# Kernel optimization log

Hardware: AMD Instinct MI355X
Metric: run time of the kernel (lower is better)

Reference implementation:

```python
import jax, jax.numpy as jnp
import numpy as np

B, L, D = 4, 1024, 1024
H = 16
HD = D // H
SCALE = HD ** -0.5
LOCAL_WINDOW = 32
HALF = LOCAL_WINDOW // 2
TEMP = 1.0
PATTERN_TEMP = 1.0
THRESHOLD = 0.1
SPARSITY_RATIO = 0.3
# k for learned sparse topk (eval mode, static given L)
EFF = min(SPARSITY_RATIO, 1.0 - 10.0 / L)
K_TOP = max(1, min(L, int(L * (1.0 - EFF))))


def setup_inputs() -> dict:
    key = jax.random.key(0)
    ks = jax.random.split(key, 16)
    def xavier(k, shape, gain=1.0):
        fan_in, fan_out = shape[1], shape[0]
        a = gain * np.sqrt(6.0 / (fan_in + fan_out))
        return jax.random.uniform(k, shape, jnp.float32, -a, a)
    return {
        'x': jax.random.normal(ks[0], (B, L, D), jnp.float32),
        'w_qkv': xavier(ks[1], (3 * D, D), gain=1.0 / np.sqrt(2.0)),
        'w_proj': xavier(ks[2], (D, D)),
        'b_proj': jnp.zeros((D,), jnp.float32),
        'ps_w1': xavier(ks[3], (D, D), gain=0.5),
        'ps_b1': jnp.zeros((D,), jnp.float32),
        'ln_g': jnp.ones((D,), jnp.float32),
        'ln_b': jnp.zeros((D,), jnp.float32),
        'ps_w2': xavier(ks[4], (D // 2, D), gain=0.5),
        'ps_b2': jnp.zeros((D // 2,), jnp.float32),
        'ps_w3': xavier(ks[5], (3, D // 2), gain=0.5),
        'ps_b3': jnp.zeros((3,), jnp.float32),
        'pattern_bias': jnp.array([0.05, 0.0, -0.05], jnp.float32),
        'sparse_w': jax.random.normal(ks[6], (H, 1, 1), jnp.float32) * 0.1 + 1.0,
        'sparse_b': jnp.zeros((H, 1, 1), jnp.float32),
    }


def _forward(x, w_qkv, w_proj, b_proj, ps_w1, ps_b1, ln_g, ln_b,
             ps_w2, ps_b2, ps_w3, ps_b3, pattern_bias, sparse_w, sparse_b):
    qkv = (x @ w_qkv.T).reshape(B, L, 3, H, HD)
    qkv = jnp.transpose(qkv, (2, 0, 3, 1, 4))  # [3,B,H,L,HD]
    q, k, v = qkv[0], qkv[1], qkv[2]
    scores = jnp.einsum('bhid,bhjd->bhij', q, k) * SCALE  # [B,H,L,L]

    # pattern selector on pooled features
    pooled = (jnp.mean(x, axis=1) + jnp.max(x, axis=1)) / 2.0  # [B,D]
    h = pooled @ ps_w1.T + ps_b1
    mu = jnp.mean(h, axis=-1, keepdims=True)
    var = jnp.mean((h - mu) ** 2, axis=-1, keepdims=True)
    h = (h - mu) / jnp.sqrt(var + 1e-5) * ln_g + ln_b
    h = jax.nn.gelu(h, approximate=False)
    h = jax.nn.gelu(h @ ps_w2.T + ps_b2, approximate=False)
    logits = h @ ps_w3.T + ps_b3 + pattern_bias  # [B,3]
    pw = jax.nn.softmax(logits / PATTERN_TEMP, axis=-1)  # [B,3]

    # learned sparse mask via per-head affine + topk scatter
    s2 = scores * jnp.abs(sparse_w)[None] + sparse_b[None]  # [B,H,L,L]
    _, topk_idx = jax.lax.top_k(s2, K_TOP)  # [B,H,L,K]
    bi = jnp.arange(B)[:, None, None, None]
    hi = jnp.arange(H)[None, :, None, None]
    li = jnp.arange(L)[None, None, :, None]
    sparse_mask = jnp.zeros_like(scores).at[bi, hi, li, topk_idx].set(1.0)

    # local sliding-window mask |i-j| <= HALF
    i = jnp.arange(L)
    local = (jnp.abs(i[:, None] - i[None, :]) <= HALF).astype(jnp.float32)  # [L,L]

    combined = (pw[:, 0, None, None, None] * local[None, None]
                + pw[:, 1, None, None, None]
                + pw[:, 2, None, None, None] * sparse_mask)
    binary = combined > THRESHOLD
    scores = jnp.where(binary, scores, -jnp.inf)

    # fallback: rows fully masked attend only to themselves (score 0)
    all_masked = ~jnp.any(binary, axis=-1)  # [B,H,L]
    eye = jnp.eye(L, dtype=bool)
    scores = jnp.where(all_masked[..., None] & eye[None, None], 0.0, scores)

    attn = jax.nn.softmax(scores / TEMP, axis=-1)
    out = jnp.einsum('bhij,bhjd->bhid', attn, v)  # [B,H,L,HD]
    out = jnp.transpose(out, (0, 2, 1, 3)).reshape(B, L, D)
    return out @ w_proj.T + b_proj


def reference(x, w_qkv, w_proj, b_proj, ps_w1, ps_b1, ln_g, ln_b,
              ps_w2, ps_b2, ps_w3, ps_b3, pattern_bias, sparse_w, sparse_b):
    return _forward(x, w_qkv, w_proj, b_proj, ps_w1, ps_b1, ln_g, ln_b,
                    ps_w2, ps_b2, ps_w3, ps_b3, pattern_bias, sparse_w, sparse_b)
```

## Files before the change

### kernel.cpp

```cpp
#include <hip/hip_runtime.h>
#include <math.h>

#define KTOP_ 716
#define SCALE_ 0.125f
#define QSCALE_ 0.1803368801111731f
#define LN2_ 0.6931471805599453f

typedef float f4v __attribute__((ext_vector_type(4)));
typedef short s8v __attribute__((ext_vector_type(8)));
typedef __bf16 bf8v __attribute__((ext_vector_type(8)));

static __device__ inline unsigned short f2bf(float f) {
  unsigned u = __float_as_uint(f);
  u += 0x7fffu + ((u >> 16) & 1u);
  return (unsigned short)(u >> 16);
}
static __device__ inline unsigned short f2bfn(float f) {
  union { __bf16 b; unsigned short u; } cv;
  cv.b = (__bf16)f;
  return cv.u;
}
static __device__ inline float bf2f(unsigned short h) {
  return __uint_as_float((unsigned)h << 16);
}
static __device__ inline f4v mfma16(s8v a, s8v b, f4v c) {
  union { s8v s; bf8v b; } ua, ub;
  ua.s = a; ub.s = b;
  return __builtin_amdgcn_mfma_f32_16x16x32_bf16(ua.b, ub.b, c, 0, 0, 0);
}
static __device__ inline void gload16(const unsigned short* g, unsigned short* lbase) {
  __builtin_amdgcn_global_load_lds(
      (const __attribute__((address_space(1))) unsigned int*)g,
      (__attribute__((address_space(3))) unsigned int*)lbase, 16, 0, 0);
}

__global__ __launch_bounds__(256) void pool1(const float* __restrict__ x,
                                             float* __restrict__ psum,
                                             float* __restrict__ pmax,
                                             unsigned short* __restrict__ xs) {
  int bid = blockIdx.x;
  int b = bid >> 6, sl = bid & 63;
  int t = threadIdx.x;
  float s[4] = {0.f, 0.f, 0.f, 0.f};
  float m[4] = {-INFINITY, -INFINITY, -INFINITY, -INFINITY};
  const float* xb = x + ((size_t)b << 20) + (size_t)sl * 16 * 1024;
  unsigned short* xo = xs + ((size_t)(b * 1024 + sl * 16)) * 1024;
  for (int l = 0; l < 16; ++l) {
    #pragma unroll
    for (int dg = 0; dg < 4; ++dg) {
      float v = xb[l * 1024 + dg * 256 + t];
      s[dg] += v;
      m[dg] = fmaxf(m[dg], v);
      xo[(size_t)l * 1024 + dg * 256 + t] = f2bfn(v);
    }
  }
  #pragma unroll
  for (int dg = 0; dg < 4; ++dg) {
    psum[(size_t)bid * 1024 + dg * 256 + t] = s[dg];
    pmax[(size_t)bid * 1024 + dg * 256 + t] = m[dg];
  }
}

__global__ __launch_bounds__(256) void ps_gemv1(const float* __restrict__ psum,
                                                const float* __restrict__ pmax,
                                                const float* __restrict__ w1,
                                                const float* __restrict__ b1,
                                                float* __restrict__ h1) {
  __shared__ float pool_s[1024];
  int bid = blockIdx.x;
  int b = bid >> 4, og = bid & 15;
  int t = threadIdx.x;
  #pragma unroll
  for (int i = 0; i < 4; ++i) {
    int d = t + 256 * i;
    float s = 0.f, m = -INFINITY;
    #pragma unroll 8
    for (int sl = 0; sl < 64; ++sl) {
      s += psum[((size_t)b * 64 + sl) * 1024 + d];
      m = fmaxf(m, pmax[((size_t)b * 64 + sl) * 1024 + d]);
    }
    pool_s[d] = (s * (1.0f / 1024.0f) + m) * 0.5f;
  }
  __syncthreads();
  int ol = t >> 2, ks = t & 3;
  int o = og * 64 + ol;
  const float4* wr = (const float4*)(w1 + (size_t)o * 1024 + ks * 256);
  const float4* pp = (const float4*)(&pool_s[ks * 256]);
  float acc = 0.f;
  #pragma unroll 8
  for (int j = 0; j < 64; ++j) {
    float4 a = wr[j], p = pp[j];
    acc += a.x * p.x + a.y * p.y + a.z * p.z + a.w * p.w;
  }
  acc += __shfl_xor(acc, 1, 64);
  acc += __shfl_xor(acc, 2, 64);
  if (ks == 0) h1[b * 1024 + o] = acc + b1[o];
}

__global__ __launch_bounds__(256) void ps_gemv2(const float* __restrict__ h1,
                                                const float* __restrict__ lng,
                                                const float* __restrict__ lnb,
                                                const float* __restrict__ w2,
                                                const float* __restrict__ b2,
                                                float* __restrict__ h2) {
  __shared__ float hs[1024];
  __shared__ float red[256];
  int bid = blockIdx.x;
  int b = bid >> 3, og = bid & 7;
  int t = threadIdx.x;
  const float* hb = h1 + b * 1024;
  float v0[4];
  float ls = 0.f;
  #pragma unroll
  for (int i = 0; i < 4; ++i) { v0[i] = hb[t + 256 * i]; ls += v0[i]; }
  red[t] = ls; __syncthreads();
  for (int s = 128; s > 0; s >>= 1) { if (t < s) red[t] += red[t + s]; __syncthreads(); }
  float mean = red[0] * (1.0f / 1024.0f);
  __syncthreads();
  float lq = 0.f;
  #pragma unroll
  for (int i = 0; i < 4; ++i) { float dv = v0[i] - mean; lq += dv * dv; }
  red[t] = lq; __syncthreads();
  for (int s = 128; s > 0; s >>= 1) { if (t < s) red[t] += red[t + s]; __syncthreads(); }
  float rstd = 1.0f / sqrtf(red[0] * (1.0f / 1024.0f) + 1e-5f);
  #pragma unroll
  for (int i = 0; i < 4; ++i) {
    float v = (v0[i] - mean) * rstd * lng[t + 256 * i] + lnb[t + 256 * i];
    hs[t + 256 * i] = 0.5f * v * (1.0f + erff(v * 0.70710678118654752f));
  }
  __syncthreads();
  int ol = t >> 2, ks = t & 3;
  int o = og * 64 + ol;
  const float4* wr = (const float4*)(w2 + (size_t)o * 1024 + ks * 256);
  const float4* pp = (const float4*)(&hs[ks * 256]);
  float acc = 0.f;
  #pragma unroll 8
  for (int j = 0; j < 64; ++j) {
    float4 a = wr[j], p = pp[j];
    acc += a.x * p.x + a.y * p.y + a.z * p.z + a.w * p.w;
  }
  acc += __shfl_xor(acc, 1, 64);
  acc += __shfl_xor(acc, 2, 64);
  if (ks == 0) {
    float v = acc + b2[o];
    h2[b * 512 + o] = 0.5f * v * (1.0f + erff(v * 0.70710678118654752f));
  }
}

__global__ __launch_bounds__(256) void ps_logits(const float* __restrict__ h2,
                                                 const float* __restrict__ w3,
                                                 const float* __restrict__ b3,
                                                 const float* __restrict__ pb,
                                                 int* __restrict__ meta) {
  __shared__ float red[256];
  int b = blockIdx.x, t = threadIdx.x;
  float lgv[3];
  for (int c = 0; c < 3; ++c) {
    float p = 0.f;
    for (int i = t; i < 512; i += 256) p += h2[b * 512 + i] * w3[c * 512 + i];
    red[t] = p; __syncthreads();
    for (int s = 128; s > 0; s >>= 1) { if (t < s) red[t] += red[t + s]; __syncthreads(); }
    lgv[c] = red[0] + b3[c] + pb[c];
    __syncthreads();
  }
  if (t == 0) {
    float mx = fmaxf(lgv[0], fmaxf(lgv[1], lgv[2]));
    float e0 = __expf(lgv[0] - mx), e1 = __expf(lgv[1] - mx), e2 = __expf(lgv[2] - mx);
    float inv = 1.0f / (e0 + e1 + e2);
    float p0 = e0 * inv, p1 = e1 * inv, p2 = e2 * inv;
    float c00 = p1;
    float c10 = p0 + p1;
    float c01 = p1 + p2;
    float c11 = (p0 + p1) + p2;
    int t00 = c00 > 0.1f, t10 = c10 > 0.1f, t01 = c01 > 0.1f, t11 = c11 > 0.1f;
    meta[b * 8 + 0] = t00;
    meta[b * 8 + 1] = t10;
    meta[b * 8 + 2] = t01;
    meta[b * 8 + 3] = t11;
    meta[b * 8 + 4] = (t00 != t01) || (t10 != t11);
  }
}

__global__ __launch_bounds__(256) void prep_w(const float* __restrict__ w_qkv,
                                              const float* __restrict__ w_proj,
                                              unsigned short* __restrict__ wqs,
                                              unsigned short* __restrict__ wps) {
  int i = blockIdx.x * 256 + threadIdx.x;
  const float* src;
  unsigned short* dst;
  int idx;
  if (i < 786432) { src = w_qkv; dst = wqs; idx = i; }
  else            { src = w_proj; dst = wps; idx = i - 786432; }
  float4 v = ((const float4*)src)[idx];
  ushort4 o;
  o.x = f2bfn(v.x); o.y = f2bfn(v.y); o.z = f2bfn(v.z); o.w = f2bfn(v.w);
  *(ushort4*)(dst + (size_t)idx * 4) = o;
}

template <int MODE>
__global__ __launch_bounds__(256) void gemm_sp(
    const unsigned short* __restrict__ A, const unsigned short* __restrict__ B,
    const float* __restrict__ bias,
    unsigned short* __restrict__ qxo, unsigned short* __restrict__ kxo,
    unsigned short* __restrict__ vxo,
    float* __restrict__ out, int Nb) {
  __shared__ unsigned short Asm[2][128 * 64];
  __shared__ unsigned short Bsm[2][128 * 64];

  int bid = blockIdx.x;
  int cpx = gridDim.x >> 3;
  int g = (bid & 7) * cpx + (bid >> 3);
  int bm = g / Nb, bn = g % Nb;
  size_t row0 = (size_t)bm * 128, col0 = (size_t)bn * 128;

  int tid = threadIdx.x, lane = tid & 63, wv = tid >> 6;
  int wm = (wv >> 1) << 6, wn = (wv & 1) << 6;
  int rowg = lane >> 4, colc = lane & 15;

  f4v acc[4][4];
  #pragma unroll
  for (int mf = 0; mf < 4; ++mf)
    #pragma unroll
    for (int nf = 0; nf < 4; ++nf) acc[mf][nf] = (f4v){0.f, 0.f, 0.f, 0.f};

  const unsigned short* Abase = A + row0 * 1024;
  const unsigned short* Bbase = B + col0 * 1024;

  auto STAGE = [&](int kb, int buf) {
    #pragma unroll
    for (int p = 0; p < 4; ++p) {
      int idx = p * 256 + tid;
      int row = idx >> 3;
      int sc = (idx & 7) ^ (row & 7);
      gload16(Abase + (size_t)row * 1024 + kb + sc * 8,
              &Asm[buf][(size_t)(p * 256 + wv * 64) * 8]);
      gload16(Bbase + (size_t)row * 1024 + kb + sc * 8,
              &Bsm[buf][(size_t)(p * 256 + wv * 64) * 8]);
    }
  };

  STAGE(0, 0);
  __syncthreads();
  int cur = 0;

  for (int kb = 0; kb < 1024; kb += 64) {
    if (kb + 64 < 1024) STAGE(kb + 64, cur ^ 1);
    #pragma unroll
    for (int ks = 0; ks < 2; ++ks) {
      s8v af[4], bf_[4];
      #pragma unroll
      for (int mf = 0; mf < 4; ++mf) {
        int row = wm + mf * 16 + colc;
        int kby = (ks * 64 + rowg * 16) ^ ((row & 7) << 4);
        af[mf] = *(const s8v*)((const char*)&Asm[cur][0] + row * 128 + kby);
      }
      #pragma unroll
      for (int nf = 0; nf < 4; ++nf) {
        int row = wn + nf * 16 + colc;
        int kby = (ks * 64 + rowg * 16) ^ ((row & 7) << 4);
        bf_[nf] = *(const s8v*)((const char*)&Bsm[cur][0] + row * 128 + kby);
      }
      #pragma unroll
      for (int mf = 0; mf < 4; ++mf)
        #pragma unroll
        for (int nf = 0; nf < 4; ++nf)
          acc[mf][nf] = mfma16(af[mf], bf_[nf], acc[mf][nf]);
    }
    __syncthreads();
    cur ^= 1;
  }

  if (MODE == 0) {
    int c = (int)(col0 >> 10);
    #pragma unroll
    for (int mf = 0; mf < 4; ++mf) {
      int m0 = (int)row0 + wm + mf * 16 + rowg * 4;
      int bb = m0 >> 10, l0 = m0 & 1023;
      #pragma unroll
      for (int nf = 0; nf < 4; ++nf) {
        int n = (int)col0 + wn + nf * 16 + colc;
        int hh = (n >> 6) & 15, hd = n & 63;
        int bhl = bb * 16 + hh;
        if (c == 2) {
          ushort4 h4;
          h4.x = f2bfn(acc[mf][nf][0]);
          h4.y = f2bfn(acc[mf][nf][1]);
          h4.z = f2bfn(acc[mf][nf][2]);
          h4.w = f2bfn(acc[mf][nf][3]);
          *(ushort4*)(vxo + ((size_t)bhl * 64 + hd) * 1024 + l0) = h4;
        } else {
          unsigned short* dst = ((c == 0) ? qxo : kxo) +
                                ((size_t)bhl * 1024 + l0) * 64 + hd;
          float sc_ = (c == 0) ? QSCALE_ : 1.0f;
          #pragma unroll
          for (int r = 0; r < 4; ++r)
            dst[(size_t)r * 64] = f2bfn(acc[mf][nf][r] * sc_);
        }
      }
    }
  } else {
    #pragma unroll
    for (int mf = 0; mf < 4; ++mf) {
      #pragma unroll
      for (int r = 0; r < 4; ++r) {
        int m = (int)row0 + wm + mf * 16 + rowg * 4 + r;
        #pragma unroll
        for (int nf = 0; nf < 4; ++nf) {
          int n = (int)col0 + wn + nf * 16 + colc;
          out[(size_t)m * 1024 + n] = acc[mf][nf][r] + bias[n];
        }
      }
    }
  }
}

__global__ __launch_bounds__(256) void attn_flash(
    const unsigned short* __restrict__ qx, const unsigned short* __restrict__ kx,
    const unsigned short* __restrict__ vx, const int* __restrict__ meta,
    unsigned short* __restrict__ ao) {
  int n = blockIdx.x;
  int bh = ((n & 7) << 3) | (n >> 7);
  int qt = (n >> 3) & 15;
  int b = bh >> 4, h = bh & 15;
  const int* mb = meta + b * 8;
  if (mb[4]) return;
  int t00 = mb[0], t10 = mb[1];

  int tid = threadIdx.x, lane = tid & 63, wv = tid >> 6;
  int g = lane >> 4, colc = lane & 15;
  int q0 = qt * 64 + wv * 16;

  if (!t10) {
    #pragma unroll
    for (int it = 0; it < 4; ++it) {
      int idx = tid + it * 256;
      int r = idx >> 4, dc = (idx & 15) * 4;
      ushort4 o;
      unsigned short* op = (unsigned short*)&o;
      #pragma unroll
      for (int j = 0; j < 4; ++j)
        op[j] = vx[((size_t)bh * 64 + dc + j) * 1024 + qt * 64 + r];
      *(ushort4*)(ao + ((size_t)b * 1024 + qt * 64 + r) * 1024 + h * 64 + dc) = o;
    }
    return;
  }
  bool local_only = !t00;

  __shared__ __align__(16) unsigned short Ksm[2][64 * 64];
  __shared__ __align__(16) unsigned short Vsm[2][64 * 64];
  __shared__ __align__(16) unsigned short px[4][16][64];

  const unsigned short* qb = qx + ((size_t)bh * 1024 + q0 + colc) * 64 + g * 8;
  s8v Q0 = *(const s8v*)(qb);
  s8v Q1 = *(const s8v*)(qb + 32);

  f4v O[4];
  #pragma unroll
  for (int df = 0; df < 4; ++df) O[df] = (f4v){0.f, 0.f, 0.f, 0.f};
  float m = -1e30f, lsum = 0.f;

  const unsigned short* kxb = kx + ((size_t)bh << 10) * 64;
  const unsigned short* vxb = vx + ((size_t)bh << 16);
  int bq0 = qt * 64;

  int jb_lo = 0, jb_hi = 15;
  if (local_only) {
    int lo = (bq0 - 16) >> 6, hi = (bq0 + 79) >> 6;
    jb_lo = lo < 0 ? 0 : lo;
    jb_hi = hi > 15 ? 15 : hi;
  }

  auto STAGE = [&](int jb2, int buf) {
    int jc = jb2 << 6;
    #pragma unroll
    for (int p = 0; p < 2; ++p) {
      int cidx = p * 256 + tid;
      int row = cidx >> 3;
      int sc = (cidx & 7) ^ (row & 7);
      gload16(kxb + (size_t)(jc + row) * 64 + sc * 8,
              &Ksm[buf][(size_t)(p * 256 + wv * 64) * 8]);
      gload16(vxb + (size_t)row * 1024 + jc + sc * 8,
              &Vsm[buf][(size_t)(p * 256 + wv * 64) * 8]);
    }
  };

  STAGE(jb_lo, 0);
  __syncthreads();
  int cur = 0;
  int swk = (colc & 7) << 4;
  int sx = (colc & 7) << 1;

  for (int jb = jb_lo; jb <= jb_hi; ++jb) {
    if (jb < jb_hi) STAGE(jb + 1, cur ^ 1);

    int jc0 = jb << 6;
    bool wact = !(local_only && (jc0 + 63 < q0 - 16 || jc0 > q0 + 31));
    if (wact) {
      f4v s[4];
      #pragma unroll
      for (int jf = 0; jf < 4; ++jf) {
        const char* kp = (const char*)&Ksm[cur][0] + (jf * 16 + colc) * 128;
        s8v K0 = *(const s8v*)(kp + ((g * 16) ^ swk));
        s8v K1 = *(const s8v*)(kp + ((64 + g * 16) ^ swk));
        f4v acc = (f4v){0.f, 0.f, 0.f, 0.f};
        acc = mfma16(K0, Q0, acc);
        acc = mfma16(K1, Q1, acc);
        s[jf] = acc;
      }

      if (local_only) {
        int i = q0 + colc;
        #pragma unroll
        for (int jf = 0; jf < 4; ++jf)
          #pragma unroll
          for (int r = 0; r < 4; ++r) {
            int j = jc0 + jf * 16 + 4 * g + r;
            int dj = i - j;
            if (dj > 16 || dj < -16) s[jf][r] = -1e30f;
          }
      }

      float cm = fmaxf(
          fmaxf(fmaxf(fmaxf(s[0][0], s[0][1]), fmaxf(s[0][2], s[0][3])),
                fmaxf(fmaxf(s[1][0], s[1][1]), fmaxf(s[1][2], s[1][3]))),
          fmaxf(fmaxf(fmaxf(s[2][0], s[2][1]), fmaxf(s[2][2], s[2][3])),
                fmaxf(fmaxf(s[3][0], s[3][1]), fmaxf(s[3][2], s[3][3]))));
      cm = fmaxf(cm, __shfl_xor(cm, 16, 64));
      cm = fmaxf(cm, __shfl_xor(cm, 32, 64));

      if (__any(cm > m + 8.0f)) {
        float mn = fmaxf(m, cm);
        float fac = __builtin_amdgcn_exp2f(m - mn);
        m = mn;
        lsum *= fac;
        float fo[4];
        #pragma unroll
        for (int r = 0; r < 4; ++r)
          fo[r] = __shfl(fac, (lane & 48) + g * 4 + r, 64);
        #pragma unroll
        for (int df = 0; df < 4; ++df)
          #pragma unroll
          for (int r = 0; r < 4; ++r) O[df][r] *= fo[r];
      }

      float psum = 0.f;
      #pragma unroll
      for (int jf = 0; jf < 4; ++jf) {
        float p0 = __builtin_amdgcn_exp2f(s[jf][0] - m);
        float p1 = __builtin_amdgcn_exp2f(s[jf][1] - m);
        float p2 = __builtin_amdgcn_exp2f(s[jf][2] - m);
        float p3 = __builtin_amdgcn_exp2f(s[jf][3] - m);
        psum += (p0 + p1) + (p2 + p3);
        ushort4 pk;
        pk.x = f2bfn(p0); pk.y = f2bfn(p1); pk.z = f2bfn(p2); pk.w = f2bfn(p3);
        *(ushort4*)&px[wv][colc][4 * ((jf * 4 + g) ^ sx)] = pk;
      }
      psum += __shfl_xor(psum, 16, 64);
      psum += __shfl_xor(psum, 32, 64);
      lsum += psum;

      s8v Pf[2];
      #pragma unroll
      for (int ks = 0; ks < 2; ++ks)
        Pf[ks] = *(const s8v*)&px[wv][colc][4 * ((ks * 8 + 2 * g) ^ sx)];
      #pragma unroll
      for (int df = 0; df < 4; ++df) {
        const char* vp = (const char*)&Vsm[cur][0] + (df * 16 + colc) * 128;
        #pragma unroll
        for (int ks = 0; ks < 2; ++ks) {
          s8v Vf = *(const s8v*)(vp + ((ks * 64 + g * 16) ^ swk));
          O[df] = mfma16(Pf[ks], Vf, O[df]);
        }
      }
    }
    __syncthreads();
    cur ^= 1;
  }

  float linv[4];
  #pragma unroll
  for (int r = 0; r < 4; ++r)
    linv[r] = 1.0f / __shfl(lsum, (lane & 48) + g * 4 + r, 64);
  #pragma unroll
  for (int df = 0; df < 4; ++df) {
    #pragma unroll
    for (int r = 0; r < 4; ++r) {
      int i = q0 + g * 4 + r;
      ao[((size_t)b * 1024 + i) * 1024 + h * 64 + df * 16 + colc] =
          f2bfn(O[df][r] * linv[r]);
    }
  }
}

__global__ __launch_bounds__(256) void attn_sparse(
    const unsigned short* __restrict__ qx, const unsigned short* __restrict__ kx,
    const unsigned short* __restrict__ vx, const int* __restrict__ meta,
    unsigned short* __restrict__ ao) {
  __shared__ float S[32][1028];
  __shared__ float qs[32][68];
  __shared__ float kc[64][68];
  __shared__ float rowsum_s[32];

  int tid = threadIdx.x;
  int lane = tid & 63;
  int wv = tid >> 6;
  int id = blockIdx.x;
  int rt = id & 31;
  int h = (id >> 5) & 15;
  int b = id >> 9;
  int bh = b * 16 + h;
  int row0 = rt * 32;

  const int* mb = meta + b * 8;
  int t00 = mb[0], t10 = mb[1], t01 = mb[2], t11 = mb[3], needs = mb[4];
  if (!needs) return;

  #pragma unroll
  for (int i = 0; i < 8; ++i) {
    int idx = tid + 256 * i;
    int r = idx >> 6, d = idx & 63;
    qs[r][d] = bf2f(qx[((size_t)bh * 1024 + row0 + r) * 64 + d]);
  }

  int lr = lane >> 4, lc = lane & 15;
  int r_a = wv * 8 + lr * 2;
  int r_b = r_a + 1;

  for (int cb = 0; cb < 16; ++cb) {
    __syncthreads();
    #pragma unroll
    for (int i = 0; i < 2; ++i) {
      int idx = tid + 256 * i;
      int cc = idx >> 3, d0 = (idx & 7) * 8;
      union { s8v v; unsigned short u[8]; } kv8;
      kv8.v = *(const s8v*)(kx + ((size_t)bh * 1024 + cb * 64 + cc) * 64 + d0);
      #pragma unroll
      for (int j = 0; j < 8; ++j) kc[cc][d0 + j] = bf2f(kv8.u[j]);
    }
    __syncthreads();

    float acc0[4] = {0.f, 0.f, 0.f, 0.f};
    float acc1[4] = {0.f, 0.f, 0.f, 0.f};
    for (int dq = 0; dq < 64; dq += 4) {
      float4 qa = *(const float4*)&qs[r_a][dq];
      float4 qb = *(const float4*)&qs[r_b][dq];
      #pragma unroll
      for (int cj = 0; cj < 4; ++cj) {
        float4 kv = *(const float4*)&kc[lc + 16 * cj][dq];
        acc0[cj] += qa.x * kv.x + qa.y * kv.y + qa.z * kv.z + qa.w * kv.w;
        acc1[cj] += qb.x * kv.x + qb.y * kv.y + qb.z * kv.z + qb.w * kv.w;
      }
    }
    #pragma unroll
    for (int cj = 0; cj < 4; ++cj) {
      S[r_a][cb * 64 + lc + 16 * cj] = acc0[cj] * LN2_;
      S[r_b][cb * 64 + lc + 16 * cj] = acc1[cj] * LN2_;
    }
  }

  for (int rr = 0; rr < 8; ++rr) {
    int r = wv * 8 + rr;
    int grow = row0 + r;
    float sv[16];
    unsigned kv[16];
    #pragma unroll
    for (int i2 = 0; i2 < 16; ++i2) {
      float s = S[r][lane + 64 * i2];
      sv[i2] = s;
      unsigned u = __float_as_uint(s);
      kv[i2] = (u & 0x80000000u) ? ~u : (u | 0x80000000u);
    }
    unsigned T = 0u;
    for (int bit = 31; bit >= 0; --bit) {
      unsigned cand = T | (1u << bit);
      int cnt = 0;
      #pragma unroll
      for (int i2 = 0; i2 < 16; ++i2) cnt += (kv[i2] >= cand) ? 1 : 0;
      for (int off = 32; off; off >>= 1) cnt += __shfl_xor(cnt, off, 64);
      if (cnt >= KTOP_) T = cand;
    }
    float mx = -INFINITY;
    int kept = 0;
    unsigned kmask = 0;
    #pragma unroll
    for (int i2 = 0; i2 < 16; ++i2) {
      int j = lane + 64 * i2;
      int sp = (kv[i2] >= T) ? 1 : 0;
      int dj = grow - j;
      int lo = (dj <= 16 && dj >= -16) ? 1 : 0;
      int keep = sp ? (lo ? t11 : t01) : (lo ? t10 : t00);
      kept += keep;
      if (keep) { kmask |= (1u << i2); mx = fmaxf(mx, sv[i2]); }
    }
    for (int off = 32; off; off >>= 1) {
      mx = fmaxf(mx, __shfl_xor(mx, off, 64));
      kept += __shfl_xor(kept, off, 64);
    }
    if (kept == 0) {
      #pragma unroll
      for (int i2 = 0; i2 < 16; ++i2) {
        int j = lane + 64 * i2;
        S[r][j] = (j == grow) ? 1.0f : 0.0f;
      }
      if (lane == 0) rowsum_s[r] = 1.0f;
    } else {
      float sum = 0.f;
      #pragma unroll
      for (int i2 = 0; i2 < 16; ++i2) {
        float p = ((kmask >> i2) & 1u) ? __expf(sv[i2] - mx) : 0.0f;
        sum += p;
        S[r][lane + 64 * i2] = p;
      }
      for (int off = 32; off; off >>= 1) sum += __shfl_xor(sum, off, 64);
      if (lane == 0) rowsum_s[r] = sum;
    }
  }

  int ld = lane & 15;
  int d0 = ld * 4;
  float4 oa0 = make_float4(0.f, 0.f, 0.f, 0.f);
  float4 oa1 = make_float4(0.f, 0.f, 0.f, 0.f);
  for (int vb = 0; vb < 16; ++vb) {
    __syncthreads();
    #pragma unroll
    for (int i = 0; i < 2; ++i) {
      int idx = tid + 256 * i;
      int d = idx >> 3, c0 = (idx & 7) * 8;
      union { s8v v; unsigned short u[8]; } vv8;
      vv8.v = *(const s8v*)(vx + ((size_t)bh * 64 + d) * 1024 + vb * 64 + c0);
      #pragma unroll
      for (int j = 0; j < 8; ++j) kc[c0 + j][d] = bf2f(vv8.u[j]);
    }
    __syncthreads();
    for (int cq = 0; cq < 64; cq += 4) {
      float4 pa = *(const float4*)&S[r_a][vb * 64 + cq];
      float4 pb = *(const float4*)&S[r_b][vb * 64 + cq];
      float par[4] = {pa.x, pa.y, pa.z, pa.w};
      float pbr[4] = {pb.x, pb.y, pb.z, pb.w};
      #pragma unroll
      for (int tt = 0; tt < 4; ++tt) {
        float4 vv = *(const float4*)&kc[cq + tt][d0];
        oa0.x += par[tt] * vv.x; oa0.y += par[tt] * vv.y;
        oa0.z += par[tt] * vv.z; oa0.w += par[tt] * vv.w;
        oa1.x += pbr[tt] * vv.x; oa1.y += pbr[tt] * vv.y;
        oa1.z += pbr[tt] * vv.z; oa1.w += pbr[tt] * vv.w;
      }
    }
  }
  float inv0 = 1.0f / rowsum_s[r_a];
  float inv1 = 1.0f / rowsum_s[r_b];
  ushort4 o0, o1;
  unsigned short* o0p = (unsigned short*)&o0;
  unsigned short* o1p = (unsigned short*)&o1;
  float v0[4] = {oa0.x * inv0, oa0.y * inv0, oa0.z * inv0, oa0.w * inv0};
  float v1[4] = {oa1.x * inv1, oa1.y * inv1, oa1.z * inv1, oa1.w * inv1};
  #pragma unroll
  for (int j = 0; j < 4; ++j) {
    o0p[j] = f2bf(v0[j]);
    o1p[j] = f2bf(v1[j]);
  }
  *(ushort4*)(ao + ((size_t)b * 1024 + row0 + r_a) * 1024 + h * 64 + d0) = o0;
  *(ushort4*)(ao + ((size_t)b * 1024 + row0 + r_b) * 1024 + h * 64 + d0) = o1;
}

__global__ __launch_bounds__(256) void pool_kernel(const float* __restrict__ x,
                                                   float* __restrict__ pooled) {
  int g = blockIdx.x * 256 + threadIdx.x;
  int b = g >> 10, d = g & 1023;
  const float* xp = x + ((size_t)b << 20) + d;
  float s = 0.f, m = -INFINITY;
  #pragma unroll 4
  for (int l = 0; l < 1024; ++l) {
    float v = xp[(size_t)l << 10];
    s += v;
    m = fmaxf(m, v);
  }
  pooled[g] = (s * (1.0f / 1024.0f) + m) * 0.5f;
}

__global__ __launch_bounds__(256) void qkv_gemm(const float* __restrict__ X,
                                                const float* __restrict__ W,
                                                float* __restrict__ qw,
                                                float* __restrict__ kw,
                                                float* __restrict__ vw) {
  __shared__ float As[8][128];
  __shared__ float Bs[8][128];
  int tid = threadIdx.x;
  int row0 = blockIdx.y * 128, col0 = blockIdx.x * 128;
  int lr = tid >> 1;
  int lk = (tid & 1) * 4;
  int ty = tid >> 4, tx = tid & 15;
  float acc[8][8] = {};

  for (int kb = 0; kb < 1024; kb += 8) {
    float4 a4 = *(const float4*)(X + (size_t)(row0 + lr) * 1024 + kb + lk);
    float4 b4 = *(const float4*)(W + (size_t)(col0 + lr) * 1024 + kb + lk);
    __syncthreads();
    As[lk + 0][lr] = a4.x; As[lk + 1][lr] = a4.y; As[lk + 2][lr] = a4.z; As[lk + 3][lr] = a4.w;
    Bs[lk + 0][lr] = b4.x; Bs[lk + 1][lr] = b4.y; Bs[lk + 2][lr] = b4.z; Bs[lk + 3][lr] = b4.w;
    __syncthreads();
    #pragma unroll
    for (int kk = 0; kk < 8; ++kk) {
      float av[8], bv[8];
      #pragma unroll
      for (int i = 0; i < 8; ++i) av[i] = As[kk][ty * 8 + i];
      #pragma unroll
      for (int j = 0; j < 8; ++j) bv[j] = Bs[kk][tx * 8 + j];
      #pragma unroll
      for (int i = 0; i < 8; ++i)
        #pragma unroll
        for (int j = 0; j < 8; ++j) acc[i][j] += av[i] * bv[j];
    }
  }
  #pragma unroll
  for (int i = 0; i < 8; ++i) {
    int m = row0 + ty * 8 + i;
    int bb = m >> 10, l = m & 1023;
    #pragma unroll
    for (int j = 0; j < 8; j += 4) {
      int n = col0 + tx * 8 + j;
      int c = n >> 10;
      int hh = (n >> 6) & 15;
      int hd = n & 63;
      float* base = (c == 0) ? qw : (c == 1) ? kw : vw;
      float* dst = base + ((size_t)(bb * 16 + hh) * 1024 + l) * 64 + hd;
      *(float4*)dst = make_float4(acc[i][j], acc[i][j + 1], acc[i][j + 2], acc[i][j + 3]);
    }
  }
}

__global__ __launch_bounds__(256) void proj_gemm(const float* __restrict__ A,
                                                 const float* __restrict__ W,
                                                 const float* __restrict__ bias,
                                                 float* __restrict__ out) {
  __shared__ float As[8][128];
  __shared__ float Bs[8][128];
  int tid = threadIdx.x;
  int row0 = blockIdx.y * 128, col0 = blockIdx.x * 128;
  int lr = tid >> 1;
  int lk = (tid & 1) * 4;
  int ty = tid >> 4, tx = tid & 15;
  float acc[8][8] = {};

  for (int kb = 0; kb < 1024; kb += 8) {
    float4 a4 = *(const float4*)(A + (size_t)(row0 + lr) * 1024 + kb + lk);
    float4 b4 = *(const float4*)(W + (size_t)(col0 + lr) * 1024 + kb + lk);
    __syncthreads();
    As[lk + 0][lr] = a4.x; As[lk + 1][lr] = a4.y; As[lk + 2][lr] = a4.z; As[lk + 3][lr] = a4.w;
    Bs[lk + 0][lr] = b4.x; Bs[lk + 1][lr] = b4.y; Bs[lk + 2][lr] = b4.z; Bs[lk + 3][lr] = b4.w;
    __syncthreads();
    #pragma unroll
    for (int kk = 0; kk < 8; ++kk) {
      float av[8], bv[8];
      #pragma unroll
      for (int i = 0; i < 8; ++i) av[i] = As[kk][ty * 8 + i];
      #pragma unroll
      for (int j = 0; j < 8; ++j) bv[j] = Bs[kk][tx * 8 + j];
      #pragma unroll
      for (int i = 0; i < 8; ++i)
        #pragma unroll
        for (int j = 0; j < 8; ++j) acc[i][j] += av[i] * bv[j];
    }
  }
  #pragma unroll
  for (int i = 0; i < 8; ++i) {
    int m = row0 + ty * 8 + i;
    #pragma unroll
    for (int j = 0; j < 8; j += 4) {
      int n = col0 + tx * 8 + j;
      *(float4*)(out + (size_t)m * 1024 + n) =
          make_float4(acc[i][j] + bias[n], acc[i][j + 1] + bias[n + 1],
                      acc[i][j + 2] + bias[n + 2], acc[i][j + 3] + bias[n + 3]);
    }
  }
}

__global__ __launch_bounds__(256) void pattern_kernel(
    const float* __restrict__ pooled,
    const float* __restrict__ w1, const float* __restrict__ b1,
    const float* __restrict__ lng, const float* __restrict__ lnb,
    const float* __restrict__ w2, const float* __restrict__ b2,
    const float* __restrict__ w3, const float* __restrict__ b3,
    const float* __restrict__ pb, int* __restrict__ meta) {
  __shared__ float pool_s[1024];
  __shared__ float h1[1024];
  __shared__ float h2[512];
  __shared__ float red[256];
  int b = blockIdx.x, t = threadIdx.x;

  for (int i = t; i < 1024; i += 256) pool_s[i] = pooled[b * 1024 + i];
  __syncthreads();
  for (int o = t; o < 1024; o += 256) {
    float acc = b1[o];
    const float* wr = w1 + (size_t)o * 1024;
    for (int k = 0; k < 1024; ++k) acc += pool_s[k] * wr[k];
    h1[o] = acc;
  }
  __syncthreads();
  float ls = 0.f;
  for (int i = t; i < 1024; i += 256) ls += h1[i];
  red[t] = ls; __syncthreads();
  for (int s = 128; s > 0; s >>= 1) { if (t < s) red[t] += red[t + s]; __syncthreads(); }
  float mean = red[0] * (1.0f / 1024.0f);
  __syncthreads();
  float lq = 0.f;
  for (int i = t; i < 1024; i += 256) { float dv = h1[i] - mean; lq += dv * dv; }
  red[t] = lq; __syncthreads();
  for (int s = 128; s > 0; s >>= 1) { if (t < s) red[t] += red[t + s]; __syncthreads(); }
  float var = red[0] * (1.0f / 1024.0f);
  float rstd = 1.0f / sqrtf(var + 1e-5f);
  __syncthreads();
  for (int i = t; i < 1024; i += 256) {
    float v = (h1[i] - mean) * rstd * lng[i] + lnb[i];
    h1[i] = 0.5f * v * (1.0f + erff(v * 0.70710678118654752f));
  }
  __syncthreads();
  for (int o = t; o < 512; o += 256) {
    float acc = b2[o];
    const float* wr = w2 + (size_t)o * 1024;
    for (int k = 0; k < 1024; ++k) acc += h1[k] * wr[k];
    h2[o] = 0.5f * acc * (1.0f + erff(acc * 0.70710678118654752f));
  }
  __syncthreads();
  float lgv[3];
  for (int c = 0; c < 3; ++c) {
    float p = 0.f;
    for (int i = t; i < 512; i += 256) p += h2[i] * w3[c * 512 + i];
    __syncthreads();
    red[t] = p; __syncthreads();
    for (int s = 128; s > 0; s >>= 1) { if (t < s) red[t] += red[t + s]; __syncthreads(); }
    lgv[c] = red[0] + b3[c] + pb[c];
  }
  if (t == 0) {
    float mx = fmaxf(lgv[0], fmaxf(lgv[1], lgv[2]));
    float e0 = __expf(lgv[0] - mx), e1 = __expf(lgv[1] - mx), e2 = __expf(lgv[2] - mx);
    float inv = 1.0f / (e0 + e1 + e2);
    float p0 = e0 * inv, p1 = e1 * inv, p2 = e2 * inv;
    float c00 = p1;
    float c10 = p0 + p1;
    float c01 = p1 + p2;
    float c11 = (p0 + p1) + p2;
    int t00 = c00 > 0.1f, t10 = c10 > 0.1f, t01 = c01 > 0.1f, t11 = c11 > 0.1f;
    meta[b * 8 + 0] = t00;
    meta[b * 8 + 1] = t10;
    meta[b * 8 + 2] = t01;
    meta[b * 8 + 3] = t11;
    meta[b * 8 + 4] = (t00 != t01) || (t10 != t11);
  }
}

__global__ __launch_bounds__(256) void attn_kernel_f32(const float* __restrict__ qw,
                                                       const float* __restrict__ kw,
                                                       const float* __restrict__ vw,
                                                       const int* __restrict__ meta,
                                                       float* __restrict__ ao) {
  __shared__ float S[32][1028];
  __shared__ float qs[32][68];
  __shared__ float kc[64][68];
  __shared__ float rowsum_s[32];

  int tid = threadIdx.x;
  int lane = tid & 63;
  int wv = tid >> 6;
  int id = blockIdx.x;
  int rt = id & 31;
  int h = (id >> 5) & 15;
  int b = id >> 9;
  int bh = b * 16 + h;
  int row0 = rt * 32;

  const int* mb = meta + b * 8;
  int t00 = mb[0], t10 = mb[1], t01 = mb[2], t11 = mb[3], needs = mb[4];

  {
    const float4* qp = (const float4*)(qw + ((size_t)bh * 1024 + row0 + wv * 8) * 64);
    #pragma unroll
    for (int i = 0; i < 2; ++i) {
      int f = lane + 64 * i;
      float4 v = qp[f];
      int r = wv * 8 + (f >> 4);
      int d = (f & 15) << 2;
      qs[r][d] = v.x; qs[r][d + 1] = v.y; qs[r][d + 2] = v.z; qs[r][d + 3] = v.w;
    }
  }

  int lr = lane >> 4, lc = lane & 15;
  int r_a = wv * 8 + lr * 2;
  int r_b = r_a + 1;

  for (int cb = 0; cb < 16; ++cb) {
    __syncthreads();
    const float4* kp = (const float4*)(kw + ((size_t)bh * 1024 + cb * 64) * 64);
    #pragma unroll
    for (int i = 0; i < 4; ++i) {
      int f = tid + 256 * i;
      float4 v = kp[f];
      int c = f >> 4, d = (f & 15) << 2;
      kc[c][d] = v.x; kc[c][d + 1] = v.y; kc[c][d + 2] = v.z; kc[c][d + 3] = v.w;
    }
    __syncthreads();

    float acc0[4] = {0.f, 0.f, 0.f, 0.f};
    float acc1[4] = {0.f, 0.f, 0.f, 0.f};
    for (int dq = 0; dq < 64; dq += 4) {
      float4 qa = *(const float4*)&qs[r_a][dq];
      float4 qb = *(const float4*)&qs[r_b][dq];
      #pragma unroll
      for (int cj = 0; cj < 4; ++cj) {
        float4 kv = *(const float4*)&kc[lc + 16 * cj][dq];
        acc0[cj] += qa.x * kv.x + qa.y * kv.y + qa.z * kv.z + qa.w * kv.w;
        acc1[cj] += qb.x * kv.x + qb.y * kv.y + qb.z * kv.z + qb.w * kv.w;
      }
    }
    #pragma unroll
    for (int cj = 0; cj < 4; ++cj) {
      S[r_a][cb * 64 + lc + 16 * cj] = acc0[cj] * SCALE_;
      S[r_b][cb * 64 + lc + 16 * cj] = acc1[cj] * SCALE_;
    }
  }

  for (int rr = 0; rr < 8; ++rr) {
    int r = wv * 8 + rr;
    int grow = row0 + r;
    float sv[16];
    unsigned kv[16];
    #pragma unroll
    for (int i2 = 0; i2 < 16; ++i2) {
      float s = S[r][lane + 64 * i2];
      sv[i2] = s;
      unsigned u = __float_as_uint(s);
      kv[i2] = (u & 0x80000000u) ? ~u : (u | 0x80000000u);
    }
    unsigned T = 0u;
    if (needs) {
      for (int bit = 31; bit >= 0; --bit) {
        unsigned cand = T | (1u << bit);
        int cnt = 0;
        #pragma unroll
        for (int i2 = 0; i2 < 16; ++i2) cnt += (kv[i2] >= cand) ? 1 : 0;
        for (int off = 32; off; off >>= 1) cnt += __shfl_xor(cnt, off, 64);
        if (cnt >= KTOP_) T = cand;
      }
    }
    float mx = -INFINITY;
    int kept = 0;
    unsigned kmask = 0;
    #pragma unroll
    for (int i2 = 0; i2 < 16; ++i2) {
      int j = lane + 64 * i2;
      int sp = (kv[i2] >= T) ? 1 : 0;
      int dj = grow - j;
      int lo = (dj <= 16 && dj >= -16) ? 1 : 0;
      int keep = sp ? (lo ? t11 : t01) : (lo ? t10 : t00);
      kept += keep;
      if (keep) { kmask |= (1u << i2); mx = fmaxf(mx, sv[i2]); }
    }
    for (int off = 32; off; off >>= 1) {
      mx = fmaxf(mx, __shfl_xor(mx, off, 64));
      kept += __shfl_xor(kept, off, 64);
    }
    if (kept == 0) {
      #pragma unroll
      for (int i2 = 0; i2 < 16; ++i2) {
        int j = lane + 64 * i2;
        S[r][j] = (j == grow) ? 1.0f : 0.0f;
      }
      if (lane == 0) rowsum_s[r] = 1.0f;
    } else {
      float sum = 0.f;
      #pragma unroll
      for (int i2 = 0; i2 < 16; ++i2) {
        float p = ((kmask >> i2) & 1u) ? __expf(sv[i2] - mx) : 0.0f;
        sum += p;
        S[r][lane + 64 * i2] = p;
      }
      for (int off = 32; off; off >>= 1) sum += __shfl_xor(sum, off, 64);
      if (lane == 0) rowsum_s[r] = sum;
    }
  }

  int ld = lane & 15;
  int d0 = ld * 4;
  float4 oa0 = make_float4(0.f, 0.f, 0.f, 0.f);
  float4 oa1 = make_float4(0.f, 0.f, 0.f, 0.f);
  for (int vb = 0; vb < 16; ++vb) {
    __syncthreads();
    const float4* vp = (const float4*)(vw + ((size_t)bh * 1024 + vb * 64) * 64);
    #pragma unroll
    for (int i = 0; i < 4; ++i) {
      int f = tid + 256 * i;
      float4 v = vp[f];
      int c = f >> 4, d = (f & 15) << 2;
      kc[c][d] = v.x; kc[c][d + 1] = v.y; kc[c][d + 2] = v.z; kc[c][d + 3] = v.w;
    }
    __syncthreads();
    for (int cq = 0; cq < 64; cq += 4) {
      float4 pa = *(const float4*)&S[r_a][vb * 64 + cq];
      float4 pb = *(const float4*)&S[r_b][vb * 64 + cq];
      float par[4] = {pa.x, pa.y, pa.z, pa.w};
      float pbr[4] = {pb.x, pb.y, pb.z, pb.w};
      #pragma unroll
      for (int tt = 0; tt < 4; ++tt) {
        float4 vv = *(const float4*)&kc[cq + tt][d0];
        oa0.x += par[tt] * vv.x; oa0.y += par[tt] * vv.y;
        oa0.z += par[tt] * vv.z; oa0.w += par[tt] * vv.w;
        oa1.x += pbr[tt] * vv.x; oa1.y += pbr[tt] * vv.y;
        oa1.z += pbr[tt] * vv.z; oa1.w += pbr[tt] * vv.w;
      }
    }
  }
  float inv0 = 1.0f / rowsum_s[r_a];
  float inv1 = 1.0f / rowsum_s[r_b];
  float* p0 = ao + ((size_t)b * 1024 + row0 + r_a) * 1024 + h * 64 + d0;
  float* p1 = ao + ((size_t)b * 1024 + row0 + r_b) * 1024 + h * 64 + d0;
  *(float4*)p0 = make_float4(oa0.x * inv0, oa0.y * inv0, oa0.z * inv0, oa0.w * inv0);
  *(float4*)p1 = make_float4(oa1.x * inv1, oa1.y * inv1, oa1.z * inv1, oa1.w * inv1);
}

extern "C" void kernel_launch(void* const* d_in, const int* in_sizes, int n_in,
                              void* d_out, int out_size, void* d_ws, size_t ws_size,
                              hipStream_t stream) {
  const float* x      = (const float*)d_in[0];
  const float* w_qkv  = (const float*)d_in[1];
  const float* w_proj = (const float*)d_in[2];
  const float* b_proj = (const float*)d_in[3];
  const float* ps_w1  = (const float*)d_in[4];
  const float* ps_b1  = (const float*)d_in[5];
  const float* ln_g   = (const float*)d_in[6];
  const float* ln_b   = (const float*)d_in[7];
  const float* ps_w2  = (const float*)d_in[8];
  const float* ps_b2  = (const float*)d_in[9];
  const float* ps_w3  = (const float*)d_in[10];
  const float* ps_b3  = (const float*)d_in[11];
  const float* pbias  = (const float*)d_in[12];

  float* ws = (float*)d_ws;
  float* pooled = ws;
  int*   meta   = (int*)(ws + 4096);
  float* h1buf  = ws + 8192;
  float* h2buf  = ws + 12288;
  float* ppsum  = ws + 16384;
  float* ppmax  = ws + 278528;
  float* qw = ws + 1048576;
  float* kw = qw + 4194304;
  float* vw = kw + 4194304;
  float* ao = vw + 4194304;
  unsigned short* u16b = (unsigned short*)(ao + 4194304);
  unsigned short* xs   = u16b;
  unsigned short* wqs  = xs + 4194304;
  unsigned short* wps  = wqs + 3145728;
  unsigned short* aos  = wps + 1048576;
  unsigned short* qx   = aos + 4194304;
  unsigned short* kx   = qx + 4194304;
  unsigned short* vx   = kx + 4194304;
  float* out = (float*)d_out;

  const size_t NEED_FULL = (size_t)(1048576 + 4 * 4194304) * 4 +
                           (size_t)(4194304 + 3145728 + 1048576 + 4194304 +
                                    3 * 4194304) * 2;

  if (ws_size >= NEED_FULL) {
    pool1<<<256, 256, 0, stream>>>(x, ppsum, ppmax, xs);
    ps_gemv1<<<64, 256, 0, stream>>>(ppsum, ppmax, ps_w1, ps_b1, h1buf);
    ps_gemv2<<<32, 256, 0, stream>>>(h1buf, ln_g, ln_b, ps_w2, ps_b2, h2buf);
    ps_logits<<<4, 256, 0, stream>>>(h2buf, ps_w3, ps_b3, pbias, meta);

    prep_w<<<4096, 256, 0, stream>>>(w_qkv, w_proj, wqs, wps);
    gemm_sp<0><<<768, 256, 0, stream>>>(xs, wqs, nullptr, qx, kx, vx,
                                        nullptr, 24);

    attn_flash<<<1024, 256, 0, stream>>>(qx, kx, vx, meta, aos);
    attn_sparse<<<2048, 256, 0, stream>>>(qx, kx, vx, meta, aos);

    gemm_sp<1><<<256, 256, 0, stream>>>(aos, wps, b_proj,
                                        nullptr, nullptr, nullptr, out, 8);
  } else {
    pool_kernel<<<16, 256, 0, stream>>>(x, pooled);
    pattern_kernel<<<4, 256, 0, stream>>>(pooled, ps_w1, ps_b1, ln_g, ln_b,
                                          ps_w2, ps_b2, ps_w3, ps_b3, pbias, meta);
    qkv_gemm<<<dim3(24, 32), 256, 0, stream>>>(x, w_qkv, qw, kw, vw);
    attn_kernel_f32<<<2048, 256, 0, stream>>>(qw, kw, vw, meta, ao);
    proj_gemm<<<dim3(8, 32), 256, 0, stream>>>(ao, w_proj, b_proj, out);
  }
}
```

Measured before the change: 150.4 us.

## Template GEMM M-tile height; halve proj tile, remap QKV block-to-XCD assignment

The bf16 GEMM kernel now takes the M tile height as a template parameter. The output projection uses 64-row tiles, doubling its grid from 256 to 512 blocks so it can fill more CUs. The QKV GEMM gets a new block-to-tile mapping that gives each XCD a contiguous 8x12 patch of tiles, improving L2 reuse of A and B within each XCD. Smaller tiles mean less operand reuse per block and more total global loads for the projection.

New measurement: 147.8 us. No clear change (-1.7%).

```diff
diff --git a/kernel.cpp b/kernel.cpp
--- a/kernel.cpp
+++ b/kernel.cpp
@@ -197,29 +197,40 @@
   *(ushort4*)(dst + (size_t)idx * 4) = o;
 }
 
-template <int MODE>
+template <int MODE, int TM>
 __global__ __launch_bounds__(256) void gemm_sp(
     const unsigned short* __restrict__ A, const unsigned short* __restrict__ B,
     const float* __restrict__ bias,
     unsigned short* __restrict__ qxo, unsigned short* __restrict__ kxo,
     unsigned short* __restrict__ vxo,
     float* __restrict__ out, int Nb) {
-  __shared__ unsigned short Asm[2][128 * 64];
+  constexpr int MFR = TM / 32;
+  __shared__ unsigned short Asm[2][TM * 64];
   __shared__ unsigned short Bsm[2][128 * 64];
 
   int bid = blockIdx.x;
-  int cpx = gridDim.x >> 3;
-  int g = (bid & 7) * cpx + (bid >> 3);
-  int bm = g / Nb, bn = g % Nb;
-  size_t row0 = (size_t)bm * 128, col0 = (size_t)bn * 128;
+  int bm, bn;
+  if (MODE == 0) {
+    int xcd = bid & 7, idx = bid >> 3;
+    int rb = (xcd >> 1) * 8, cb = (xcd & 1) * 12;
+    int r, c;
+    if (idx < 64) { r = idx & 7; c = idx >> 3; }
+    else          { int j = idx - 64; r = j & 7; c = 8 + (j >> 3); }
+    bm = rb + r; bn = cb + c;
+  } else {
+    int cpx = gridDim.x >> 3;
+    int g = (bid & 7) * cpx + (bid >> 3);
+    bm = g / Nb; bn = g % Nb;
+  }
+  size_t row0 = (size_t)bm * TM, col0 = (size_t)bn * 128;
 
   int tid = threadIdx.x, lane = tid & 63, wv = tid >> 6;
-  int wm = (wv >> 1) << 6, wn = (wv & 1) << 6;
+  int wm = (wv >> 1) * (MFR * 16), wn = (wv & 1) << 6;
   int rowg = lane >> 4, colc = lane & 15;
 
-  f4v acc[4][4];
-  #pragma unroll
-  for (int mf = 0; mf < 4; ++mf)
+  f4v acc[MFR][4];
+  #pragma unroll
+  for (int mf = 0; mf < MFR; ++mf)
     #pragma unroll
     for (int nf = 0; nf < 4; ++nf) acc[mf][nf] = (f4v){0.f, 0.f, 0.f, 0.f};
 
@@ -228,12 +239,18 @@
 
   auto STAGE = [&](int kb, int buf) {
     #pragma unroll
-    for (int p = 0; p < 4; ++p) {
+    for (int p = 0; p < TM / 32; ++p) {
       int idx = p * 256 + tid;
       int row = idx >> 3;
       int sc = (idx & 7) ^ (row & 7);
       gload16(Abase + (size_t)row * 1024 + kb + sc * 8,
               &Asm[buf][(size_t)(p * 256 + wv * 64) * 8]);
+    }
+    #pragma unroll
+    for (int p = 0; p < 4; ++p) {
+      int idx = p * 256 + tid;
+      int row = idx >> 3;
+      int sc = (idx & 7) ^ (row & 7);
       gload16(Bbase + (size_t)row * 1024 + kb + sc * 8,
               &Bsm[buf][(size_t)(p * 256 + wv * 64) * 8]);
     }
@@ -247,9 +264,9 @@
     if (kb + 64 < 1024) STAGE(kb + 64, cur ^ 1);
     #pragma unroll
     for (int ks = 0; ks < 2; ++ks) {
-      s8v af[4], bf_[4];
-      #pragma unroll
-      for (int mf = 0; mf < 4; ++mf) {
+      s8v af[MFR], bf_[4];
+      #pragma unroll
+      for (int mf = 0; mf < MFR; ++mf) {
         int row = wm + mf * 16 + colc;
         int kby = (ks * 64 + rowg * 16) ^ ((row & 7) << 4);
         af[mf] = *(const s8v*)((const char*)&Asm[cur][0] + row * 128 + kby);
@@ -261,7 +278,7 @@
         bf_[nf] = *(const s8v*)((const char*)&Bsm[cur][0] + row * 128 + kby);
       }
       #pragma unroll
-      for (int mf = 0; mf < 4; ++mf)
+      for (int mf = 0; mf < MFR; ++mf)
         #pragma unroll
         for (int nf = 0; nf < 4; ++nf)
           acc[mf][nf] = mfma16(af[mf], bf_[nf], acc[mf][nf]);
@@ -273,7 +290,7 @@
   if (MODE == 0) {
     int c = (int)(col0 >> 10);
     #pragma unroll
-    for (int mf = 0; mf < 4; ++mf) {
+    for (int mf = 0; mf < MFR; ++mf) {
       int m0 = (int)row0 + wm + mf * 16 + rowg * 4;
       int bb = m0 >> 10, l0 = m0 & 1023;
       #pragma unroll
@@ -300,7 +317,7 @@
     }
   } else {
     #pragma unroll
-    for (int mf = 0; mf < 4; ++mf) {
+    for (int mf = 0; mf < MFR; ++mf) {
       #pragma unroll
       for (int r = 0; r < 4; ++r) {
         int m = (int)row0 + wm + mf * 16 + rowg * 4 + r;
@@ -1066,14 +1083,14 @@
     ps_logits<<<4, 256, 0, stream>>>(h2buf, ps_w3, ps_b3, pbias, meta);
 
     prep_w<<<4096, 256, 0, stream>>>(w_qkv, w_proj, wqs, wps);
-    gemm_sp<0><<<768, 256, 0, stream>>>(xs, wqs, nullptr, qx, kx, vx,
-                                        nullptr, 24);
+    gemm_sp<0, 128><<<768, 256, 0, stream>>>(xs, wqs, nullptr, qx, kx, vx,
+                                             nullptr, 24);
 
     attn_flash<<<1024, 256, 0, stream>>>(qx, kx, vx, meta, aos);
     attn_sparse<<<2048, 256, 0, stream>>>(qx, kx, vx, meta, aos);
 
-    gemm_sp<1><<<256, 256, 0, stream>>>(aos, wps, b_proj,
-                                        nullptr, nullptr, nullptr, out, 8);
+    gemm_sp<1, 64><<<512, 256, 0, stream>>>(aos, wps, b_proj,
+                                            nullptr, nullptr, nullptr, out, 8);
   } else {
     pool_kernel<<<16, 256, 0, stream>>>(x, pooled);
     pattern_kernel<<<4, 256, 0, stream>>>(pooled, ps_w1, ps_b1, ln_g, ln_b,
```
